# Optimization experiments

Measured on AMD Instinct MI355X. Metric: run time of the kernel, lower is better.

## Reference

```python
import jax, jax.numpy as jnp
import numpy as np

N_TOKENS = 32768
D_MODEL = 1024


def setup_inputs() -> dict:
    key = jax.random.key(0)
    kx, kr, kw1, kb1, kw2, kb2 = jax.random.split(key, 6)
    scale = 1.0 / np.sqrt(D_MODEL)
    x = jax.random.normal(kx, (N_TOKENS, D_MODEL), dtype=jnp.float32)
    # RandomScatterRouter: each token independently routed to one of 2 experts
    route = jax.random.randint(kr, (N_TOKENS,), 0, 2, dtype=jnp.int32)
    W1 = jax.random.normal(kw1, (D_MODEL, D_MODEL), dtype=jnp.float32) * scale
    b1 = jax.random.normal(kb1, (D_MODEL,), dtype=jnp.float32) * scale
    W2 = jax.random.normal(kw2, (D_MODEL, D_MODEL), dtype=jnp.float32) * scale
    b2 = jax.random.normal(kb2, (D_MODEL,), dtype=jnp.float32) * scale
    return {"x": x, "W1": W1, "b1": b1, "W2": W2, "b2": b2, "route": route}


def reference(x, W1, b1, W2, b2, route):
    # Semantics of scatter -> expert linears -> gather(reverse_indice):
    #   out[i] = x[i] @ W_{route[i]} + b_{route[i]}  (original token order restored)
    # jit-friendly form: mask-partition tokens to each expert (m0 + m1 == 1),
    # run the two expert GEMMs on the disjoint partitions, sum to recombine.
    m0 = (route == 0).astype(x.dtype)[:, None]  # [N, 1]
    m1 = 1.0 - m0
    y0 = (x * m0) @ W1 + b1 * m0  # expert-1 output on its tokens, zeros elsewhere
    y1 = (x * m1) @ W2 + b2 * m1  # expert-2 output on its tokens, zeros elsewhere
    return y0 + y1
```

## Files before the change

### kernel.cpp

```cpp
#include <hip/hip_runtime.h>

#define NT 32768
#define DM 1024
#define NTOT (NT + 128)

typedef __bf16 bf16x8 __attribute__((ext_vector_type(8)));
typedef float f32x4 __attribute__((ext_vector_type(4)));

#define GLD16(g, l)                                                            \
  __builtin_amdgcn_global_load_lds(                                            \
      (const __attribute__((address_space(1))) void*)(g),                      \
      (__attribute__((address_space(3))) void*)(l), 16, 0, 0)

__device__ __forceinline__ unsigned short f2bf(float f) {
  unsigned u = __float_as_uint(f);
  u += 0x7fffu + ((u >> 16) & 1u);
  return (unsigned short)(u >> 16);
}

__global__ __launch_bounds__(256) void prep_k(
    const float* __restrict__ x, unsigned short* __restrict__ xb,
    const float* __restrict__ W1, const float* __restrict__ W2,
    unsigned short* __restrict__ Wt,
    const int* __restrict__ route, int* __restrict__ idx,
    int* __restrict__ counters) {
  __shared__ float tile[32][33];
  __shared__ int wsum[4];
  const int bid = blockIdx.x;
  const int t = threadIdx.x;

  if (bid == 0) {
    const int lane = t & 63, wv = t >> 6;
    const int base = t * 128;
    const int4* rp = (const int4*)(route + base);
    unsigned m[4] = {0u, 0u, 0u, 0u};
#pragma unroll
    for (int v = 0; v < 32; ++v) {
      int4 q = rp[v];
      const int g = v >> 3, sh = (v & 7) * 4;
      m[g] |= (unsigned)(q.x == 0) << (sh + 0);
      m[g] |= (unsigned)(q.y == 0) << (sh + 1);
      m[g] |= (unsigned)(q.z == 0) << (sh + 2);
      m[g] |= (unsigned)(q.w == 0) << (sh + 3);
    }
    const int c0 = __popc(m[0]) + __popc(m[1]) + __popc(m[2]) + __popc(m[3]);
    int s = c0;
#pragma unroll
    for (int d = 1; d < 64; d <<= 1) {
      int v = __shfl_up(s, (unsigned)d, 64);
      if (lane >= d) s += v;
    }
    if (lane == 63) wsum[wv] = s;
    __syncthreads();
    int waveBase = 0, total0 = 0;
#pragma unroll
    for (int w = 0; w < 4; ++w) {
      int v = wsum[w];
      if (w < wv) waveBase += v;
      total0 += v;
    }
    const int ex0 = waveBase + s - c0;
    int slot0 = ex0;
    int slot1 = NTOT - 1 - (base - ex0);
    for (int i = 0; i < 128; ++i) {
      int token = base + i;
      if ((m[i >> 5] >> (i & 31)) & 1) idx[slot0++] = token;
      else                             idx[slot1--] = token;
    }
    if (t == 0) { counters[0] = total0; counters[1] = NT - total0; }
  } else if (bid <= 2048) {
    const int b = bid - 1;
    const int z = b >> 10;
    const int bb = b & 1023;
    const float* __restrict__ W = z ? W2 : W1;
    unsigned short* __restrict__ dst = Wt + (size_t)z * DM * DM;
    const int n0 = (bb & 31) * 32, k0 = (bb >> 5) * 32;
    const int tx = t & 31, ty = t >> 5;
#pragma unroll
    for (int i = 0; i < 32; i += 8)
      tile[ty + i][tx] = W[(size_t)(k0 + ty + i) * DM + n0 + tx];
    __syncthreads();
#pragma unroll
    for (int i = 0; i < 32; i += 8)
      dst[(size_t)(n0 + ty + i) * DM + k0 + tx] = f2bf(tile[tx][ty + i]);
  } else {
    const size_t p = (size_t)(bid - 2049) * 256 + t;
    float4 v0 = ((const float4*)x)[2 * p];
    float4 v1 = ((const float4*)x)[2 * p + 1];
    bf16x8 pk;
    pk[0] = (__bf16)v0.x; pk[1] = (__bf16)v0.y;
    pk[2] = (__bf16)v0.z; pk[3] = (__bf16)v0.w;
    pk[4] = (__bf16)v1.x; pk[5] = (__bf16)v1.y;
    pk[6] = (__bf16)v1.z; pk[7] = (__bf16)v1.w;
    ((bf16x8*)xb)[p] = pk;
  }
}

__global__ __launch_bounds__(256, 4) void gemm_k(
    const unsigned short* __restrict__ xb,
    const unsigned short* __restrict__ Wt,
    const float* __restrict__ b1, const float* __restrict__ b2,
    const int* __restrict__ idx, const int* __restrict__ counters,
    float* __restrict__ out) {
  __shared__ unsigned short As[128 * 64];
  __shared__ unsigned short Bs[128 * 64];

  const int t = threadIdx.x;
  const int lane = t & 63, wave = t >> 6;

  const int lin = blockIdx.y * 8 + blockIdx.x;
  const int L = (lin & 7) * 257 + (lin >> 3);
  const int row0 = (L >> 3) * 128;
  const int col0 = (L & 7) * 128;
  const int ph = (L >> 3) & 15;

  const int n0 = counters[0];
  const int expert = (row0 < n0) ? 0 : 1;
  const unsigned short* Wte = Wt + (size_t)expert * DM * DM;
  const float* bias = expert ? b2 : b1;

  const int wr = (wave >> 1) * 64;
  const int wc = (wave & 1) * 64;
  const int lr = lane & 15;

  const int rsub = t >> 3;
  const int cA = ((t & 7) ^ (rsub & 7)) * 8;
  const unsigned short* aSrc[4];
  const unsigned short* bSrc[4];
#pragma unroll
  for (int p = 0; p < 4; ++p) {
    int gr = row0 + p * 32 + rsub;
    int tok = idx[gr];
    if (gr >= n0 && gr < n0 + 128) tok = 0;
    aSrc[p] = xb + (size_t)tok * DM + cA;
    bSrc[p] = Wte + (size_t)(col0 + p * 32 + rsub) * DM + cA;
  }

  f32x4 acc[4][4] = {};

  for (int kt = 0; kt < 16; ++kt) {
    const int k0 = ((kt + ph) & 15) * 64;
#pragma unroll
    for (int p = 0; p < 4; ++p) {
      int q = p * 256 + t;
      GLD16(aSrc[p] + k0, As + q * 8);
      GLD16(bSrc[p] + k0, Bs + q * 8);
    }
    __syncthreads();
#pragma unroll
    for (int s = 0; s < 2; ++s) {
      const int cb = s * 4 + (lane >> 4);
      bf16x8 af[4], bfr[4];
#pragma unroll
      for (int i = 0; i < 4; ++i) {
        int r = wr + i * 16 + lr;
        af[i] = *(const bf16x8*)&As[(r * 8 + (cb ^ (r & 7))) * 8];
      }
#pragma unroll
      for (int j = 0; j < 4; ++j) {
        int r = wc + j * 16 + lr;
        bfr[j] = *(const bf16x8*)&Bs[(r * 8 + (cb ^ (r & 7))) * 8];
      }
#pragma unroll
      for (int i = 0; i < 4; ++i)
#pragma unroll
        for (int j = 0; j < 4; ++j)
          acc[i][j] = __builtin_amdgcn_mfma_f32_16x16x32_bf16(af[i], bfr[j], acc[i][j], 0, 0, 0);
    }
    __syncthreads();
  }

#pragma unroll
  for (int i = 0; i < 4; ++i) {
#pragma unroll
    for (int reg = 0; reg < 4; ++reg) {
      int gr = row0 + wr + i * 16 + (lane >> 4) * 4 + reg;
      if (gr < n0 || gr >= n0 + 128) {
        int dest = idx[gr];
#pragma unroll
        for (int j = 0; j < 4; ++j) {
          int gc = col0 + wc + j * 16 + (lane & 15);
          out[(size_t)dest * DM + gc] = acc[i][j][reg] + bias[gc];
        }
      }
    }
  }
}

extern "C" void kernel_launch(void* const* d_in, const int* in_sizes, int n_in,
                              void* d_out, int out_size, void* d_ws, size_t ws_size,
                              hipStream_t stream) {
  const float* x   = (const float*)d_in[0];
  const float* W1  = (const float*)d_in[1];
  const float* b1  = (const float*)d_in[2];
  const float* W2  = (const float*)d_in[3];
  const float* b2  = (const float*)d_in[4];
  const int*   route = (const int*)d_in[5];
  float* out = (float*)d_out;

  char* ws = (char*)d_ws;
  unsigned short* xb = (unsigned short*)ws;
  size_t off = (size_t)NT * DM * 2;
  unsigned short* Wt = (unsigned short*)(ws + off);
  off += (size_t)2 * DM * DM * 2;
  int* idx = (int*)(ws + off);
  int* counters = idx + NTOT;

  prep_k<<<18433, 256, 0, stream>>>(x, xb, W1, W2, Wt, route, idx, counters);
  gemm_k<<<dim3(8, NTOT / 128), 256, 0, stream>>>(xb, Wt, b1, b2, idx, counters, out);
}
```

Baseline: 329.5 us.

## Fuse x fp32-to-bf16 conversion into GEMM A-tile loads

Removes the separate pass that converts x to bf16 in the prep kernel. The GEMM now streams fp32 x rows directly into LDS with a new swizzle and converts them to bf16 while building fragments. This drops a 128MB read plus 64MB write round trip, but the GEMM reads x in fp32 once per column tile (8x), uses twice the LDS for A, and runs at lower occupancy.

```diff
diff --git a/kernel.cpp b/kernel.cpp
--- a/kernel.cpp
+++ b/kernel.cpp
@@ -19,7 +19,6 @@
 }
 
 __global__ __launch_bounds__(256) void prep_k(
-    const float* __restrict__ x, unsigned short* __restrict__ xb,
     const float* __restrict__ W1, const float* __restrict__ W2,
     unsigned short* __restrict__ Wt,
     const int* __restrict__ route, int* __restrict__ idx,
@@ -68,7 +67,7 @@
       else                             idx[slot1--] = token;
     }
     if (t == 0) { counters[0] = total0; counters[1] = NT - total0; }
-  } else if (bid <= 2048) {
+  } else {
     const int b = bid - 1;
     const int z = b >> 10;
     const int bb = b & 1023;
@@ -83,26 +82,16 @@
 #pragma unroll
     for (int i = 0; i < 32; i += 8)
       dst[(size_t)(n0 + ty + i) * DM + k0 + tx] = f2bf(tile[tx][ty + i]);
-  } else {
-    const size_t p = (size_t)(bid - 2049) * 256 + t;
-    float4 v0 = ((const float4*)x)[2 * p];
-    float4 v1 = ((const float4*)x)[2 * p + 1];
-    bf16x8 pk;
-    pk[0] = (__bf16)v0.x; pk[1] = (__bf16)v0.y;
-    pk[2] = (__bf16)v0.z; pk[3] = (__bf16)v0.w;
-    pk[4] = (__bf16)v1.x; pk[5] = (__bf16)v1.y;
-    pk[6] = (__bf16)v1.z; pk[7] = (__bf16)v1.w;
-    ((bf16x8*)xb)[p] = pk;
-  }
-}
-
-__global__ __launch_bounds__(256, 4) void gemm_k(
-    const unsigned short* __restrict__ xb,
+  }
+}
+
+__global__ __launch_bounds__(256, 3) void gemm_k(
+    const float* __restrict__ x,
     const unsigned short* __restrict__ Wt,
     const float* __restrict__ b1, const float* __restrict__ b2,
     const int* __restrict__ idx, const int* __restrict__ counters,
     float* __restrict__ out) {
-  __shared__ unsigned short As[128 * 64];
+  __shared__ float As[128 * 64];
   __shared__ unsigned short Bs[128 * 64];
 
   const int t = threadIdx.x;
@@ -123,43 +112,57 @@
   const int wc = (wave & 1) * 64;
   const int lr = lane & 15;
 
-  const int rsub = t >> 3;
-  const int cA = ((t & 7) ^ (rsub & 7)) * 8;
-  const unsigned short* aSrc[4];
-  const unsigned short* bSrc[4];
-#pragma unroll
-  for (int p = 0; p < 4; ++p) {
-    int gr = row0 + p * 32 + rsub;
+  const int lA = t & 15;
+  const int keyA = (t >> 4) & 7;
+  const int gA = (lA & 8) | ((lA & 7) ^ keyA);
+  const float* aSrc[8];
+#pragma unroll
+  for (int p = 0; p < 8; ++p) {
+    int gr = row0 + p * 16 + (t >> 4);
     int tok = idx[gr];
     if (gr >= n0 && gr < n0 + 128) tok = 0;
-    aSrc[p] = xb + (size_t)tok * DM + cA;
-    bSrc[p] = Wte + (size_t)(col0 + p * 32 + rsub) * DM + cA;
-  }
+    aSrc[p] = x + (size_t)tok * DM + gA * 4;
+  }
+  const int rsubB = t >> 3;
+  const int cB = ((t & 7) ^ (rsubB & 7)) * 8;
+  const unsigned short* bSrc[4];
+#pragma unroll
+  for (int p = 0; p < 4; ++p)
+    bSrc[p] = Wte + (size_t)(col0 + p * 32 + rsubB) * DM + cB;
 
   f32x4 acc[4][4] = {};
 
   for (int kt = 0; kt < 16; ++kt) {
     const int k0 = ((kt + ph) & 15) * 64;
 #pragma unroll
-    for (int p = 0; p < 4; ++p) {
-      int q = p * 256 + t;
-      GLD16(aSrc[p] + k0, As + q * 8);
-      GLD16(bSrc[p] + k0, Bs + q * 8);
-    }
+    for (int p = 0; p < 8; ++p)
+      GLD16(aSrc[p] + k0, As + (p * 256 + t) * 4);
+#pragma unroll
+    for (int p = 0; p < 4; ++p)
+      GLD16(bSrc[p] + k0, Bs + (p * 256 + t) * 8);
     __syncthreads();
 #pragma unroll
     for (int s = 0; s < 2; ++s) {
-      const int cb = s * 4 + (lane >> 4);
+      const int cb8 = s * 4 + (lane >> 4);
+      const int g0 = 2 * cb8;
       bf16x8 af[4], bfr[4];
 #pragma unroll
       for (int i = 0; i < 4; ++i) {
         int r = wr + i * 16 + lr;
-        af[i] = *(const bf16x8*)&As[(r * 8 + (cb ^ (r & 7))) * 8];
+        int l0 = (g0 & 8) | ((g0 & 7) ^ (r & 7));
+        f32x4 f0 = *(const f32x4*)&As[(r * 16 + l0) * 4];
+        f32x4 f1 = *(const f32x4*)&As[(r * 16 + (l0 ^ 1)) * 4];
+        bf16x8 a;
+        a[0] = (__bf16)f0[0]; a[1] = (__bf16)f0[1];
+        a[2] = (__bf16)f0[2]; a[3] = (__bf16)f0[3];
+        a[4] = (__bf16)f1[0]; a[5] = (__bf16)f1[1];
+        a[6] = (__bf16)f1[2]; a[7] = (__bf16)f1[3];
+        af[i] = a;
       }
 #pragma unroll
       for (int j = 0; j < 4; ++j) {
         int r = wc + j * 16 + lr;
-        bfr[j] = *(const bf16x8*)&Bs[(r * 8 + (cb ^ (r & 7))) * 8];
+        bfr[j] = *(const bf16x8*)&Bs[(r * 8 + (cb8 ^ (r & 7))) * 8];
       }
 #pragma unroll
       for (int i = 0; i < 4; ++i)
@@ -199,13 +202,11 @@
   float* out = (float*)d_out;
 
   char* ws = (char*)d_ws;
-  unsigned short* xb = (unsigned short*)ws;
-  size_t off = (size_t)NT * DM * 2;
-  unsigned short* Wt = (unsigned short*)(ws + off);
-  off += (size_t)2 * DM * DM * 2;
+  unsigned short* Wt = (unsigned short*)ws;
+  size_t off = (size_t)2 * DM * DM * 2;
   int* idx = (int*)(ws + off);
   int* counters = idx + NTOT;
 
-  prep_k<<<18433, 256, 0, stream>>>(x, xb, W1, W2, Wt, route, idx, counters);
-  gemm_k<<<dim3(8, NTOT / 128), 256, 0, stream>>>(xb, Wt, b1, b2, idx, counters, out);
-}
+  prep_k<<<2049, 256, 0, stream>>>(W1, W2, Wt, route, idx, counters);
+  gemm_k<<<dim3(8, NTOT / 128), 256, 0, stream>>>(x, Wt, b1, b2, idx, counters, out);
+}
```

Result: slower. 358.4 us (+8.8%).
